# Optimization experiments

Hardware: AMD Instinct MI355X
Metric: run time of the kernel (lower is better)

## Reference

```python
import jax, jax.numpy as jnp
import numpy as np

B, T, H = 16, 2048, 1024
L_ORDER, R_ORDER = 1, 1
K = L_ORDER + R_ORDER + 1
THRESH = 1.0


def _alphas(hidden, conv_w, conv_b, lin_w, lin_b):
    # hidden: [B, T, H]
    context = jnp.swapaxes(hidden, 1, 2)  # [B, H, T]
    q = jnp.pad(context, ((0, 0), (0, 0), (L_ORDER, R_ORDER)))  # ConstantPad1d
    mem = jax.lax.conv_general_dilated(
        q, conv_w, (1,), 'VALID',
        dimension_numbers=('NCH', 'OIH', 'NCH'),
        feature_group_count=conv_w.shape[0])  # depthwise conv, groups=idim
    mem = mem + conv_b[None, :, None]
    out = jnp.swapaxes(mem + context, 1, 2)  # [B, T, H] (dropout = identity, eval)
    out = jax.nn.relu(out)
    out = out @ lin_w.T + lin_b  # [B, T, 1]
    return jax.nn.sigmoid(out)[..., 0]  # [B, T]


def _cif_scan(hidden, alphas, threshold):
    # sequential integrate-and-fire over time, vectorized over batch via lax.scan
    b, t, h = hidden.shape

    def step(carry, xs):
        integrate, frame = carry          # [B], [B, H]
        alpha, h_t = xs                   # [B], [B, H]
        dist = 1.0 - integrate            # distribution_completion
        integrate = integrate + alpha
        fires_t = integrate
        fire = integrate >= threshold
        integrate = jnp.where(fire, integrate - 1.0, integrate)
        cur = jnp.where(fire, dist, alpha)
        rem = alpha - cur
        frame = frame + cur[:, None] * h_t
        frames_t = frame
        frame = jnp.where(fire[:, None], rem[:, None] * h_t, frame)
        return (integrate, frame), (fires_t, frames_t)

    init = (jnp.zeros((b,), hidden.dtype), jnp.zeros((b, h), hidden.dtype))
    xs = (jnp.swapaxes(alphas, 0, 1), jnp.swapaxes(hidden, 0, 1))
    _, (fires, frames) = jax.lax.scan(step, init, xs)
    return jnp.swapaxes(frames, 0, 1), jnp.swapaxes(fires, 0, 1)  # [B,T,H], [B,T]


def _gather_fired(frames, fires, threshold, max_label_len):
    # per-batch select frames where fires>=threshold, pad to max_label_len
    b, t, h = frames.shape
    mask = fires >= threshold                         # [B, T]
    rank = jnp.cumsum(mask.astype(jnp.int32), axis=1) - 1
    idx = jnp.where(mask, rank, max_label_len)        # invalid -> dummy row
    out = jnp.zeros((b, max_label_len + 1, h), frames.dtype)
    out = out.at[jnp.arange(b)[:, None], idx].add(
        jnp.where(mask[..., None], frames, 0.0))
    return out[:, :max_label_len]


def setup_inputs() -> dict:
    key = jax.random.key(0)
    k1, k2, k3, k4 = jax.random.split(key, 4)
    hidden = jax.random.normal(k1, (B, T, H), jnp.float32)
    conv_w = jax.random.normal(k2, (H, 1, K), jnp.float32) / np.sqrt(K)
    conv_b = jax.random.normal(k3, (H,), jnp.float32) * 0.01
    lin_w = jax.random.normal(k4, (1, H), jnp.float32) / np.sqrt(H)
    lin_b = jnp.zeros((1,), jnp.float32)
    return {"hidden": hidden, "conv_w": conv_w, "conv_b": conv_b,
            "lin_w": lin_w, "lin_b": lin_b}


def reference(hidden, conv_w, conv_b, lin_w, lin_b):
    alphas = _alphas(hidden, conv_w, conv_b, lin_w, lin_b)  # [B, T]
    cif_length = alphas.sum(-1)                             # [B]
    frames, fires = _cif_scan(hidden, alphas, THRESH)
    # data-dependent output length (matches torch: round(alphas.sum(-1)).max())
    max_label_len = int(jnp.round(cif_length).astype(jnp.int32).max())
    cif_output = _gather_fired(frames, fires, THRESH, max_label_len)
    return cif_output, cif_length, fires
```

## Files before the change

kernel.cpp:

```cpp
#include <hip/hip_runtime.h>
#include <math.h>

#define B_ 16
#define T_ 2048
#define H_ 1024
#define TPB 16
#define KPB 8

__global__ __launch_bounds__(256) void k1_alphas(
    const float* __restrict__ hidden, const float* __restrict__ conv_w,
    const float* __restrict__ conv_b, const float* __restrict__ lin_w,
    const float* __restrict__ lin_b, float* __restrict__ alphas)
{
    const int tile = blockIdx.x & (T_ / TPB - 1);
    const int b    = blockIdx.x / (T_ / TPB);
    const int tid  = threadIdx.x;
    const int h0   = tid * 4;

    float w0[4], w1[4], w2[4];
    {
        const float4* cw = (const float4*)(conv_w + (size_t)h0 * 3);
        float4 c0 = cw[0], c1 = cw[1], c2 = cw[2];
        w0[0] = c0.x; w1[0] = c0.y; w2[0] = c0.z;
        w0[1] = c0.w; w1[1] = c1.x; w2[1] = c1.y;
        w0[2] = c1.z; w1[2] = c1.w; w2[2] = c2.x;
        w0[3] = c2.y; w1[3] = c2.z; w2[3] = c2.w;
    }
    const float4 cb = *(const float4*)(conv_b + h0);
    const float4 lw = *(const float4*)(lin_w + h0);
    const float  lb = lin_b[0];

    const size_t base = ((size_t)b * T_) * H_ + h0;
    const int t0 = tile * TPB;

    float4 prev = (t0 > 0) ? *(const float4*)(hidden + base + (size_t)(t0 - 1) * H_)
                           : make_float4(0.f, 0.f, 0.f, 0.f);
    float4 curr = *(const float4*)(hidden + base + (size_t)t0 * H_);
    float4 next;

    __shared__ float lds[4][TPB];
    const int wave = tid >> 6;
    const int lane = tid & 63;

    #pragma unroll
    for (int tt = 0; tt < TPB; ++tt) {
        const int t = t0 + tt;
        next = (t + 1 < T_) ? *(const float4*)(hidden + base + (size_t)(t + 1) * H_)
                            : make_float4(0.f, 0.f, 0.f, 0.f);
        float p = 0.f, v;
        v = fmaf(w0[0], prev.x, fmaf(w1[0], curr.x, fmaf(w2[0], next.x, cb.x + curr.x)));
        p = fmaf(fmaxf(v, 0.f), lw.x, p);
        v = fmaf(w0[1], prev.y, fmaf(w1[1], curr.y, fmaf(w2[1], next.y, cb.y + curr.y)));
        p = fmaf(fmaxf(v, 0.f), lw.y, p);
        v = fmaf(w0[2], prev.z, fmaf(w1[2], curr.z, fmaf(w2[2], next.z, cb.z + curr.z)));
        p = fmaf(fmaxf(v, 0.f), lw.z, p);
        v = fmaf(w0[3], prev.w, fmaf(w1[3], curr.w, fmaf(w2[3], next.w, cb.w + curr.w)));
        p = fmaf(fmaxf(v, 0.f), lw.w, p);
        #pragma unroll
        for (int m = 32; m; m >>= 1) p += __shfl_xor(p, m);
        if (lane == 0) lds[wave][tt] = p;
        prev = curr; curr = next;
    }
    __syncthreads();
    if (tid < TPB) {
        float s = lds[0][tid] + lds[1][tid] + lds[2][tid] + lds[3][tid] + lb;
        alphas[(size_t)b * T_ + t0 + tid] = 1.f / (1.f + expf(-s));
    }
}

__global__ __launch_bounds__(256) void k2_scan_coef(
    const float* __restrict__ alphas, float* __restrict__ fires,
    float* __restrict__ cur, float* __restrict__ rem,
    int* __restrict__ fire_pos, int* __restrict__ n_fires,
    float* __restrict__ cif_length, int Lpad)
{
    const int b = blockIdx.x;
    const int tid = threadIdx.x;
    const size_t base = (size_t)b * T_;

    __shared__ float sA[T_];
    __shared__ float sF[T_];

    {
        const int i = tid * 8;
        *(float4*)(sA + i)     = *(const float4*)(alphas + base + i);
        *(float4*)(sA + i + 4) = *(const float4*)(alphas + base + i + 4);
    }
    __syncthreads();

    if (tid == 0) {
        float I = 0.f;
        for (int t = 0; t < T_; t += 8) {
            #pragma unroll
            for (int j = 0; j < 8; ++j) {
                I += sA[t + j];
                sF[t + j] = I;
                I = __builtin_amdgcn_fractf(I);
            }
        }
    }
    __syncthreads();

    const int t0 = tid * 8;
    float a[8], f[8];
    #pragma unroll
    for (int j = 0; j < 8; ++j) { a[j] = sA[t0 + j]; f[j] = sF[t0 + j]; }
    const float fprev = (t0 == 0) ? 0.f : sF[t0 - 1];

    *(float4*)(fires + base + t0)     = make_float4(f[0], f[1], f[2], f[3]);
    *(float4*)(fires + base + t0 + 4) = make_float4(f[4], f[5], f[6], f[7]);

    float cu[8], re[8];
    bool fr[8];
    float asum = 0.f;
    int cnt = 0;
    #pragma unroll
    for (int j = 0; j < 8; ++j) {
        float fp = (j == 0) ? fprev : f[j - 1];
        float Iprev = __builtin_amdgcn_fractf(fp);
        fr[j] = (f[j] >= 1.f);
        const float dist = 1.f - Iprev;
        cu[j] = fr[j] ? dist : a[j];
        re[j] = a[j] - cu[j];
        cnt += fr[j] ? 1 : 0;
        asum += a[j];
    }
    *(float4*)(cur + base + t0)     = *(float4*)(cu);
    *(float4*)(cur + base + t0 + 4) = *(float4*)(cu + 4);
    *(float4*)(rem + base + t0)     = *(float4*)(re);
    *(float4*)(rem + base + t0 + 4) = *(float4*)(re + 4);

    const int lane = tid & 63, wave = tid >> 6;
    int inc = cnt;
    #pragma unroll
    for (int d = 1; d < 64; d <<= 1) {
        int v = __shfl_up(inc, d);
        if (lane >= d) inc += v;
    }
    __shared__ int wsum[4];
    if (lane == 63) wsum[wave] = inc;
    __syncthreads();
    int waveoff = 0;
    for (int w = 0; w < wave; ++w) waveoff += wsum[w];
    int r = waveoff + inc - cnt;
    #pragma unroll
    for (int j = 0; j < 8; ++j) {
        if (fr[j]) {
            if (r < Lpad) fire_pos[b * Lpad + r] = t0 + j;
            ++r;
        }
    }
    if (tid == 255) n_fires[b] = waveoff + inc;

    float s = asum;
    #pragma unroll
    for (int m = 32; m; m >>= 1) s += __shfl_xor(s, m);
    __shared__ float wred[4];
    if (lane == 0) wred[wave] = s;
    __syncthreads();
    if (tid == 0) cif_length[b] = wred[0] + wred[1] + wred[2] + wred[3];
}

__global__ __launch_bounds__(256) void k3_frames(
    const float* __restrict__ hidden, const float* __restrict__ cur,
    const float* __restrict__ rem, const int* __restrict__ fire_pos,
    const int* __restrict__ n_fires, float* __restrict__ out,
    int L, int Lpad)
{
    const int k0 = blockIdx.x * KPB;
    const int b  = blockIdx.y;
    const int tid = threadIdx.x;
    const int h0 = tid * 4;
    const int n = n_fires[b];
    const size_t hb = ((size_t)b * T_) * H_ + h0;
    const size_t cb = (size_t)b * T_;

    int s = -1;
    float4 hprev = make_float4(0.f, 0.f, 0.f, 0.f);
    if (k0 > 0) {
        s = fire_pos[b * Lpad + k0 - 1];
        if (k0 < n)
            hprev = *(const float4*)(hidden + hb + (size_t)s * H_);
    }

    #pragma unroll 1
    for (int kk = 0; kk < KPB; ++kk) {
        const int k = k0 + kk;
        if (k >= L) break;
        float4 acc = make_float4(0.f, 0.f, 0.f, 0.f);
        if (k < n) {
            const int e = fire_pos[b * Lpad + k];
            if (k > 0) {
                const float w = rem[cb + s];
                acc.x = w * hprev.x; acc.y = w * hprev.y;
                acc.z = w * hprev.z; acc.w = w * hprev.w;
            }
            for (int t = s + 1; t < e; ++t) {
                const float w = cur[cb + t];
                const float4 hr = *(const float4*)(hidden + hb + (size_t)t * H_);
                acc.x = fmaf(w, hr.x, acc.x); acc.y = fmaf(w, hr.y, acc.y);
                acc.z = fmaf(w, hr.z, acc.z); acc.w = fmaf(w, hr.w, acc.w);
            }
            {
                const float w = cur[cb + e];
                const float4 hr = *(const float4*)(hidden + hb + (size_t)e * H_);
                acc.x = fmaf(w, hr.x, acc.x); acc.y = fmaf(w, hr.y, acc.y);
                acc.z = fmaf(w, hr.z, acc.z); acc.w = fmaf(w, hr.w, acc.w);
                hprev = hr;
            }
            s = e;
        }
        *(float4*)(out + ((size_t)b * L + k) * H_ + h0) = acc;
    }
}

extern "C" void kernel_launch(void* const* d_in, const int* in_sizes, int n_in,
                              void* d_out, int out_size, void* d_ws, size_t ws_size,
                              hipStream_t stream) {
    const float* hidden = (const float*)d_in[0];
    const float* conv_w = (const float*)d_in[1];
    const float* conv_b = (const float*)d_in[2];
    const float* lin_w  = (const float*)d_in[3];
    const float* lin_b  = (const float*)d_in[4];
    float* out = (float*)d_out;

    const int L = (out_size - B_ - B_ * T_) / (B_ * H_);
    float* cif_output = out;
    float* cif_length = out + (size_t)B_ * L * H_;
    float* fires      = cif_length + B_;

    float* alphas = (float*)d_ws;
    float* cur    = alphas + (size_t)B_ * T_;
    float* rem    = cur + (size_t)B_ * T_;
    const int Lpad = L + 8;
    int* fire_pos = (int*)(rem + (size_t)B_ * T_);
    int* n_fires  = fire_pos + (size_t)B_ * Lpad;

    k1_alphas<<<dim3(B_ * (T_ / TPB)), 256, 0, stream>>>(
        hidden, conv_w, conv_b, lin_w, lin_b, alphas);
    k2_scan_coef<<<dim3(B_), 256, 0, stream>>>(
        alphas, fires, cur, rem, fire_pos, n_fires, cif_length, Lpad);
    k3_frames<<<dim3((L + KPB - 1) / KPB, B_), 256, 0, stream>>>(
        hidden, cur, rem, fire_pos, n_fires, cif_output, L, Lpad);
}
```

Measured before the change: 262.3 us.

## Flatten frame accumulation into single software-pipelined loop with interleaved weights

Interleaves cur and rem into one float2 weight array, with rem set to -1 on non-fire steps to serve as the fire flag. The frame kernel then walks the time range of its eight output frames in one flat loop and emits a frame whenever the flag is non-negative. It prefetches hidden rows two steps ahead to hide load latency and uses readfirstlane to keep indices uniform. This removes the per-frame loop restarts, the separate fire_pos reads and the serialized load-then-FMA chains, at the cost of more registers.

```diff
diff --git a/kernel.cpp b/kernel.cpp
--- a/kernel.cpp
+++ b/kernel.cpp
@@ -70,7 +70,7 @@
 
 __global__ __launch_bounds__(256) void k2_scan_coef(
     const float* __restrict__ alphas, float* __restrict__ fires,
-    float* __restrict__ cur, float* __restrict__ rem,
+    float* __restrict__ wgt,
     int* __restrict__ fire_pos, int* __restrict__ n_fires,
     float* __restrict__ cif_length, int Lpad)
 {
@@ -110,7 +110,7 @@
     *(float4*)(fires + base + t0)     = make_float4(f[0], f[1], f[2], f[3]);
     *(float4*)(fires + base + t0 + 4) = make_float4(f[4], f[5], f[6], f[7]);
 
-    float cu[8], re[8];
+    float w[16];
     bool fr[8];
     float asum = 0.f;
     int cnt = 0;
@@ -120,15 +120,20 @@
         float Iprev = __builtin_amdgcn_fractf(fp);
         fr[j] = (f[j] >= 1.f);
         const float dist = 1.f - Iprev;
-        cu[j] = fr[j] ? dist : a[j];
-        re[j] = a[j] - cu[j];
+        const float cu = fr[j] ? dist : a[j];
+        const float re = a[j] - cu;
+        w[2 * j]     = cu;
+        w[2 * j + 1] = fr[j] ? re : -1.f;
         cnt += fr[j] ? 1 : 0;
         asum += a[j];
     }
-    *(float4*)(cur + base + t0)     = *(float4*)(cu);
-    *(float4*)(cur + base + t0 + 4) = *(float4*)(cu + 4);
-    *(float4*)(rem + base + t0)     = *(float4*)(re);
-    *(float4*)(rem + base + t0 + 4) = *(float4*)(re + 4);
+    {
+        const size_t wb = ((size_t)b * T_ + t0) * 2;
+        *(float4*)(wgt + wb)      = *(float4*)(w);
+        *(float4*)(wgt + wb + 4)  = *(float4*)(w + 4);
+        *(float4*)(wgt + wb + 8)  = *(float4*)(w + 8);
+        *(float4*)(wgt + wb + 12) = *(float4*)(w + 12);
+    }
 
     const int lane = tid & 63, wave = tid >> 6;
     int inc = cnt;
@@ -141,7 +146,7 @@
     if (lane == 63) wsum[wave] = inc;
     __syncthreads();
     int waveoff = 0;
-    for (int w = 0; w < wave; ++w) waveoff += wsum[w];
+    for (int w2 = 0; w2 < wave; ++w2) waveoff += wsum[w2];
     int r = waveoff + inc - cnt;
     #pragma unroll
     for (int j = 0; j < 8; ++j) {
@@ -162,56 +167,75 @@
 }
 
 __global__ __launch_bounds__(256) void k3_frames(
-    const float* __restrict__ hidden, const float* __restrict__ cur,
-    const float* __restrict__ rem, const int* __restrict__ fire_pos,
-    const int* __restrict__ n_fires, float* __restrict__ out,
-    int L, int Lpad)
+    const float* __restrict__ hidden, const float* __restrict__ wgt,
+    const int* __restrict__ fire_pos, const int* __restrict__ n_fires,
+    float* __restrict__ out, int L, int Lpad)
 {
     const int k0 = blockIdx.x * KPB;
     const int b  = blockIdx.y;
     const int tid = threadIdx.x;
     const int h0 = tid * 4;
-    const int n = n_fires[b];
     const size_t hb = ((size_t)b * T_) * H_ + h0;
-    const size_t cb = (size_t)b * T_;
-
-    int s = -1;
-    float4 hprev = make_float4(0.f, 0.f, 0.f, 0.f);
+    const float2* wb = (const float2*)wgt + (size_t)b * T_;
+
+    const int n = __builtin_amdgcn_readfirstlane(n_fires[b]);
+    const int kmax = min(KPB, L - k0);
+    const int kact = min(kmax, n - k0);
+
+    const float4 zero4 = make_float4(0.f, 0.f, 0.f, 0.f);
+    if (kact <= 0) {
+        for (int kk = 0; kk < kmax; ++kk)
+            *(float4*)(out + ((size_t)b * L + (k0 + kk)) * H_ + h0) = zero4;
+        return;
+    }
+
+    const int tend = __builtin_amdgcn_readfirstlane(fire_pos[b * Lpad + k0 + kact - 1]);
+
+    float4 acc;
+    int t;
     if (k0 > 0) {
-        s = fire_pos[b * Lpad + k0 - 1];
-        if (k0 < n)
-            hprev = *(const float4*)(hidden + hb + (size_t)s * H_);
-    }
-
-    #pragma unroll 1
-    for (int kk = 0; kk < KPB; ++kk) {
-        const int k = k0 + kk;
-        if (k >= L) break;
-        float4 acc = make_float4(0.f, 0.f, 0.f, 0.f);
-        if (k < n) {
-            const int e = fire_pos[b * Lpad + k];
-            if (k > 0) {
-                const float w = rem[cb + s];
-                acc.x = w * hprev.x; acc.y = w * hprev.y;
-                acc.z = w * hprev.z; acc.w = w * hprev.w;
-            }
-            for (int t = s + 1; t < e; ++t) {
-                const float w = cur[cb + t];
-                const float4 hr = *(const float4*)(hidden + hb + (size_t)t * H_);
-                acc.x = fmaf(w, hr.x, acc.x); acc.y = fmaf(w, hr.y, acc.y);
-                acc.z = fmaf(w, hr.z, acc.z); acc.w = fmaf(w, hr.w, acc.w);
-            }
-            {
-                const float w = cur[cb + e];
-                const float4 hr = *(const float4*)(hidden + hb + (size_t)e * H_);
-                acc.x = fmaf(w, hr.x, acc.x); acc.y = fmaf(w, hr.y, acc.y);
-                acc.z = fmaf(w, hr.z, acc.z); acc.w = fmaf(w, hr.w, acc.w);
-                hprev = hr;
-            }
-            s = e;
+        const int s0 = __builtin_amdgcn_readfirstlane(fire_pos[b * Lpad + k0 - 1]);
+        const float4 hr = *(const float4*)(hidden + hb + (size_t)s0 * H_);
+        const float rm = wb[s0].y;
+        acc.x = rm * hr.x; acc.y = rm * hr.y; acc.z = rm * hr.z; acc.w = rm * hr.w;
+        t = s0 + 1;
+    } else {
+        acc = zero4;
+        t = 0;
+    }
+
+    float4 hA, hB, hC;
+    float2 wA, wB, wC;
+    hA = *(const float4*)(hidden + hb + (size_t)t * H_);
+    wA = wb[t];
+    if (t + 1 <= tend) {
+        hB = *(const float4*)(hidden + hb + (size_t)(t + 1) * H_);
+        wB = wb[t + 1];
+    } else { hB = zero4; wB = make_float2(0.f, -1.f); }
+
+    int kk = 0;
+    while (t <= tend) {
+        if (t + 2 <= tend) {
+            hC = *(const float4*)(hidden + hb + (size_t)(t + 2) * H_);
+            wC = wb[t + 2];
+        } else { hC = zero4; wC = make_float2(0.f, -1.f); }
+
+        acc.x = fmaf(wA.x, hA.x, acc.x);
+        acc.y = fmaf(wA.x, hA.y, acc.y);
+        acc.z = fmaf(wA.x, hA.z, acc.z);
+        acc.w = fmaf(wA.x, hA.w, acc.w);
+        if (wA.y >= 0.f) {
+            *(float4*)(out + ((size_t)b * L + (k0 + kk)) * H_ + h0) = acc;
+            acc.x = wA.y * hA.x; acc.y = wA.y * hA.y;
+            acc.z = wA.y * hA.z; acc.w = wA.y * hA.w;
+            ++kk;
         }
-        *(float4*)(out + ((size_t)b * L + k) * H_ + h0) = acc;
-    }
+        hA = hB; wA = wB; hB = hC; wB = wC;
+        ++t;
+    }
+
+    for (; kk < kmax; ++kk)
+        *(float4*)(out + ((size_t)b * L + (k0 + kk)) * H_ + h0) = zero4;
 }
 
 extern "C" void kernel_launch(void* const* d_in, const int* in_sizes, int n_in,
@@ -230,16 +254,15 @@
     float* fires      = cif_length + B_;
 
     float* alphas = (float*)d_ws;
-    float* cur    = alphas + (size_t)B_ * T_;
-    float* rem    = cur + (size_t)B_ * T_;
+    float* wgt    = alphas + (size_t)B_ * T_;
     const int Lpad = L + 8;
-    int* fire_pos = (int*)(rem + (size_t)B_ * T_);
+    int* fire_pos = (int*)(wgt + (size_t)2 * B_ * T_);
     int* n_fires  = fire_pos + (size_t)B_ * Lpad;
 
     k1_alphas<<<dim3(B_ * (T_ / TPB)), 256, 0, stream>>>(
         hidden, conv_w, conv_b, lin_w, lin_b, alphas);
     k2_scan_coef<<<dim3(B_), 256, 0, stream>>>(
-        alphas, fires, cur, rem, fire_pos, n_fires, cif_length, Lpad);
+        alphas, fires, wgt, fire_pos, n_fires, cif_length, Lpad);
     k3_frames<<<dim3((L + KPB - 1) / KPB, B_), 256, 0, stream>>>(
-        hidden, cur, rem, fire_pos, n_fires, cif_output, L, Lpad);
-}
+        hidden, wgt, fire_pos, n_fires, cif_output, L, Lpad);
+}
```

Result: no change. 261.8 us (-0.2%).
